# Performance work log

Measured on AMD Instinct MI355X. Metric: run time of the kernel, lower is better.

Reference implementation:

```python
import jax, jax.numpy as jnp
import numpy as np

EMBED_DIM = 4096
NUM_HEADS = 32
HEAD_DIM = EMBED_DIM // NUM_HEADS  # 128
KV_LEN = 8192


def setup_inputs() -> dict:
    key = jax.random.key(0)
    ks = jax.random.split(key, 12)
    s = 1.0 / np.sqrt(EMBED_DIM)
    return {
        "x": jax.random.normal(ks[0], (EMBED_DIM,), jnp.float32),
        "v": jax.random.normal(ks[1], (KV_LEN, NUM_HEADS, HEAD_DIM), jnp.float32),
        "k": jax.random.normal(ks[2], (KV_LEN, NUM_HEADS, HEAD_DIM), jnp.float32),
        "Wv": jax.random.normal(ks[3], (EMBED_DIM, EMBED_DIM), jnp.float32) * s,
        "bv": jnp.zeros((EMBED_DIM,), jnp.float32),
        "Wq": jax.random.normal(ks[4], (EMBED_DIM, EMBED_DIM), jnp.float32) * s,
        "bq": jnp.zeros((EMBED_DIM,), jnp.float32),
        "Wk": jax.random.normal(ks[5], (EMBED_DIM, EMBED_DIM), jnp.float32) * s,
        "bk": jnp.zeros((EMBED_DIM,), jnp.float32),
        "Wo": jax.random.normal(ks[6], (EMBED_DIM, EMBED_DIM), jnp.float32) * s,
        "bo": jnp.zeros((EMBED_DIM,), jnp.float32),
    }


def reference(x, v, k, Wv, bv, Wq, bq, Wk, bk, Wo, bo):
    # Project the single incoming token to q/k/v heads.
    v_i = (x @ Wv + bv).reshape(1, NUM_HEADS, HEAD_DIM)
    q_i = (x @ Wq + bq).reshape(NUM_HEADS, HEAD_DIM)
    k_i = (x @ Wk + bk).reshape(1, NUM_HEADS, HEAD_DIM)
    # Rolling cache: drop oldest slot, append new token.
    v = jnp.concatenate((v[1:], v_i), axis=0)  # [KV_LEN, H, D]
    k = jnp.concatenate((k[1:], k_i), axis=0)
    # Valid slots are those with any nonzero value entry.
    mask = jnp.any(v != 0, axis=(1, 2))  # [KV_LEN]
    attn = jnp.einsum('hd,khd->hk', q_i, k) / jnp.sqrt(jnp.float32(HEAD_DIM))
    attn = jnp.where(mask, attn, -jnp.inf)
    attn = jax.nn.softmax(attn, axis=-1)  # [H, KV_LEN]
    values = jnp.einsum('hk,khd->hd', attn, v).reshape(EMBED_DIM)
    out_i = values @ Wo + bo
    return (out_i, v, k)
```

## Files before the change

### kernel.cpp

```cpp
#include <hip/hip_runtime.h>

#define E 4096
#define H 32
#define L 8192
#define SCALE 0.08838834764831845f

typedef float fv4 __attribute__((ext_vector_type(4)));

__device__ __forceinline__ fv4 ntload4(const float* p) {
  return __builtin_nontemporal_load(reinterpret_cast<const fv4*>(p));
}
__device__ __forceinline__ void ntstore4(float* p, fv4 v) {
  __builtin_nontemporal_store(v, reinterpret_cast<fv4*>(p));
}

__global__ __launch_bounds__(256) void zero_ws(float* __restrict__ ws, int n) {
  int i = blockIdx.x * 256 + threadIdx.x;
  if (i < n) ws[i] = 0.f;
}

__global__ __launch_bounds__(256) void gemv_qkv(const float* __restrict__ x,
    const float* __restrict__ Wq, const float* __restrict__ Wk,
    const float* __restrict__ Wv, float* __restrict__ qacc,
    float* __restrict__ kacc, float* __restrict__ vacc) {
  int b = blockIdx.x;
  int mat = b >> 7;
  int rem = b & 127;
  int chunk = rem >> 2;
  int g = rem & 3;
  const float* W = (mat == 0) ? Wq : (mat == 1) ? Wk : Wv;
  float* accb = (mat == 0) ? qacc : (mat == 1) ? kacc : vacc;
  int rep = (b >> 2) & 3;
  float* acc = accb + (rep << 12);
  int t = threadIdx.x;
  int j = (g << 10) + (t << 2);
  float ax = 0.f, ay = 0.f, az = 0.f, aw = 0.f;
  int i0 = chunk << 7;
  #pragma unroll 8
  for (int r = 0; r < 128; ++r) {
    int i = i0 + r;
    float xi = x[i];
    const fv4 w4 = ntload4(W + (size_t)i * E + j);
    ax += xi * w4.x; ay += xi * w4.y; az += xi * w4.z; aw += xi * w4.w;
  }
  atomicAdd(acc + j + 0, ax);
  atomicAdd(acc + j + 1, ay);
  atomicAdd(acc + j + 2, az);
  atomicAdd(acc + j + 3, aw);
}

__device__ __forceinline__ void load_slot(int o, int t,
    const float* __restrict__ kin, const float* __restrict__ vin,
    const float* __restrict__ kacc, const float* __restrict__ vacc,
    const float* __restrict__ bk, const float* __restrict__ bv,
    fv4 k4[4], fv4 v4[4]) {
  if (o < L - 1) {
    const float* ks = kin + (size_t)(o + 1) * E;
    const float* vs = vin + (size_t)(o + 1) * E;
    #pragma unroll
    for (int c = 0; c < 4; ++c) {
      int e = (c << 10) + (t << 2);
      k4[c] = ntload4(ks + e);
      v4[c] = ntload4(vs + e);
    }
  } else {
    #pragma unroll
    for (int c = 0; c < 4; ++c) {
      int e = (c << 10) + (t << 2);
      fv4 ka = *reinterpret_cast<const fv4*>(kacc + e);
      fv4 va = *reinterpret_cast<const fv4*>(vacc + e);
      #pragma unroll
      for (int r = 1; r < 4; ++r) {
        ka += *reinterpret_cast<const fv4*>(kacc + (r << 12) + e);
        va += *reinterpret_cast<const fv4*>(vacc + (r << 12) + e);
      }
      k4[c] = ka + *reinterpret_cast<const fv4*>(bk + e);
      v4[c] = va + *reinterpret_cast<const fv4*>(bv + e);
    }
  }
}

template<int NSLOTS, bool PARTIAL>
__global__ __launch_bounds__(256) void kvpass(const float* __restrict__ kin,
    const float* __restrict__ vin,
    const float* __restrict__ bq, const float* __restrict__ bk,
    const float* __restrict__ bv,
    const float* __restrict__ qacc, const float* __restrict__ kacc,
    const float* __restrict__ vacc,
    float* __restrict__ kout, float* __restrict__ vout,
    float* __restrict__ nump, float* __restrict__ denp) {
  __shared__ float wlds[NSLOTS * 32];
  __shared__ int flags[NSLOTS];
  int t = threadIdx.x;
  for (int s = t; s < NSLOTS; s += 256) flags[s] = 0;
  fv4 q4[4];
  #pragma unroll
  for (int c = 0; c < 4; ++c) {
    int e = (c << 10) + (t << 2);
    fv4 qa = *reinterpret_cast<const fv4*>(qacc + e);
    #pragma unroll
    for (int r = 1; r < 4; ++r)
      qa += *reinterpret_cast<const fv4*>(qacc + (r << 12) + e);
    q4[c] = qa + *reinterpret_cast<const fv4*>(bq + e);
  }
  __syncthreads();

  float accx[4] = {0,0,0,0}, accy[4] = {0,0,0,0};
  float accz[4] = {0,0,0,0}, accw[4] = {0,0,0,0};
  int base = blockIdx.x * NSLOTS;

  fv4 kc[4], vc[4], kn[4], vn[4];
  load_slot(base, t, kin, vin, kacc, vacc, bk, bv, kc, vc);

  for (int s = 0; s < NSLOTS; ++s) {
    int o = base + s;
    if (s + 1 < NSLOTS)
      load_slot(o + 1, t, kin, vin, kacc, vacc, bk, bv, kn, vn);
    float* kd = kout + (size_t)o * E;
    float* vd = vout + (size_t)o * E;
    #pragma unroll
    for (int c = 0; c < 4; ++c) {
      int e = (c << 10) + (t << 2);
      ntstore4(kd + e, kc[c]);
      ntstore4(vd + e, vc[c]);
    }
    bool nz = false;
    #pragma unroll
    for (int c = 0; c < 4; ++c) {
      float pp = kc[c].x * q4[c].x + kc[c].y * q4[c].y +
                 kc[c].z * q4[c].z + kc[c].w * q4[c].w;
      #pragma unroll
      for (int off = 16; off >= 1; off >>= 1)
        pp += __shfl_xor(pp, off);
      float w = __expf(pp * SCALE);
      accx[c] += w * vc[c].x; accy[c] += w * vc[c].y;
      accz[c] += w * vc[c].z; accw[c] += w * vc[c].w;
      if ((t & 31) == 0) wlds[(s << 5) + (c << 3) + (t >> 5)] = w;
      nz = nz || vc[c].x != 0.f || vc[c].y != 0.f || vc[c].z != 0.f || vc[c].w != 0.f;
    }
    unsigned long long b = __ballot(nz);
    if ((t & 63) == 0 && b != 0ULL) atomicOr(&flags[s], 1);
    #pragma unroll
    for (int c = 0; c < 4; ++c) { kc[c] = kn[c]; vc[c] = vn[c]; }
  }
  if (PARTIAL) {
    float* np = nump + ((size_t)blockIdx.x << 12);
    #pragma unroll
    for (int c = 0; c < 4; ++c) {
      int e = (c << 10) + (t << 2);
      fv4 val = {accx[c], accy[c], accz[c], accw[c]};
      *reinterpret_cast<fv4*>(np + e) = val;
    }
  } else {
    float* np = nump + ((size_t)(blockIdx.x & 15) << 12);
    #pragma unroll
    for (int c = 0; c < 4; ++c) {
      int e = (c << 10) + (t << 2);
      atomicAdd(np + e + 0, accx[c]);
      atomicAdd(np + e + 1, accy[c]);
      atomicAdd(np + e + 2, accz[c]);
      atomicAdd(np + e + 3, accw[c]);
    }
  }
  __syncthreads();
  if (t < 32) {
    float d = 0.f;
    #pragma unroll
    for (int s = 0; s < NSLOTS; ++s)
      if (flags[s]) d += wlds[(s << 5) + t];
    if (PARTIAL) denp[blockIdx.x * 64 + t] = d;
    else atomicAdd(denp + (blockIdx.x & 15) * 64 + t, d);
  }
}

template<int NP>
__global__ __launch_bounds__(256) void merge(const float* __restrict__ nump,
    const float* __restrict__ denp, float* __restrict__ num,
    float* __restrict__ den) {
  int b = blockIdx.x;
  int t = threadIdx.x;
  if (b < 16) {
    int e = b * 256 + t;
    float s = 0.f;
    #pragma unroll 8
    for (int p = 0; p < NP; ++p) s += nump[((size_t)p << 12) + e];
    num[e] = s;
  } else {
    __shared__ float dl[8][32];
    int g = t >> 5, h = t & 31;
    float d = 0.f;
    for (int p = g; p < NP; p += 8) d += denp[p * 64 + h];
    dl[g][h] = d;
    __syncthreads();
    if (t < 32) {
      float s = 0.f;
      #pragma unroll
      for (int g2 = 0; g2 < 8; ++g2) s += dl[g2][t];
      den[t] = s;
    }
  }
}

__global__ __launch_bounds__(256) void gemv_out(const float* __restrict__ Wo,
    const float* __restrict__ bo, const float* __restrict__ num,
    const float* __restrict__ den, float* __restrict__ opart) {
  int b = blockIdx.x;
  int chunk = b >> 2;
  int g = b & 3;
  int t = threadIdx.x;
  int j = (g << 10) + (t << 2);
  __shared__ float vals[64];
  int i0 = chunk << 6;
  if (t < 64) vals[t] = num[i0 + t] / den[(i0 + t) >> 7];
  __syncthreads();
  float ax = 0.f, ay = 0.f, az = 0.f, aw = 0.f;
  #pragma unroll 4
  for (int r = 0; r < 64; ++r) {
    int i = i0 + r;
    float vi = vals[r];
    const fv4 w4 = ntload4(Wo + (size_t)i * E + j);
    ax += vi * w4.x; ay += vi * w4.y; az += vi * w4.z; aw += vi * w4.w;
  }
  if (chunk == 0) {
    const fv4 b4 = *reinterpret_cast<const fv4*>(bo + j);
    ax += b4.x; ay += b4.y; az += b4.z; aw += b4.w;
  }
  fv4 val = {ax, ay, az, aw};
  *reinterpret_cast<fv4*>(opart + (chunk << 12) + j) = val;
}

__global__ __launch_bounds__(256) void writeout(const float* __restrict__ opart,
                                                float* __restrict__ out) {
  int i = blockIdx.x * 256 + threadIdx.x;
  float s = 0.f;
  #pragma unroll 8
  for (int c = 0; c < 64; ++c) s += opart[(c << 12) + i];
  out[i] = s;
}

extern "C" void kernel_launch(void* const* d_in, const int* in_sizes, int n_in,
                              void* d_out, int out_size, void* d_ws, size_t ws_size,
                              hipStream_t stream) {
  const float* x   = (const float*)d_in[0];
  const float* vin = (const float*)d_in[1];
  const float* kin = (const float*)d_in[2];
  const float* Wv  = (const float*)d_in[3];
  const float* bv  = (const float*)d_in[4];
  const float* Wq  = (const float*)d_in[5];
  const float* bq  = (const float*)d_in[6];
  const float* Wk  = (const float*)d_in[7];
  const float* bk  = (const float*)d_in[8];
  const float* Wo  = (const float*)d_in[9];
  const float* bo  = (const float*)d_in[10];
  float* out  = (float*)d_out;
  float* vout = out + E;
  float* kout = vout + (size_t)L * E;
  float* ws   = (float*)d_ws;

  float* qacc = ws;
  float* kacc = ws + 16384;
  float* vacc = ws + 32768;
  const size_t bigFloats = 49152 + (size_t)256 * 4096 + 256 * 64 + 4096 + 64
                         + (size_t)64 * 4096;
  bool big = ws_size >= bigFloats * sizeof(float);

  float *nump, *denp, *num, *den, *opart;
  int zcount;
  if (big) {
    nump = ws + 49152;
    denp = nump + (size_t)256 * 4096;
    num  = denp + 256 * 64;
    den  = num + 4096;
    opart = den + 64;
    zcount = 49152;
  } else {
    nump = ws + 49152;
    denp = nump + 16 * 4096;
    num  = denp + 16 * 64;
    den  = num + 4096;
    opart = den + 64;
    zcount = 49152 + 16 * 4096 + 16 * 64;
  }

  zero_ws<<<(zcount + 255) / 256, 256, 0, stream>>>(ws, zcount);
  gemv_qkv<<<384, 256, 0, stream>>>(x, Wq, Wk, Wv, qacc, kacc, vacc);
  if (big) {
    kvpass<32, true><<<L / 32, 256, 0, stream>>>(kin, vin, bq, bk, bv,
        qacc, kacc, vacc, kout, vout, nump, denp);
    merge<256><<<17, 256, 0, stream>>>(nump, denp, num, den);
  } else {
    kvpass<16, false><<<L / 16, 256, 0, stream>>>(kin, vin, bq, bk, bv,
        qacc, kacc, vacc, kout, vout, nump, denp);
    merge<16><<<17, 256, 0, stream>>>(nump, denp, num, den);
  }
  gemv_out<<<256, 256, 0, stream>>>(Wo, bo, num, den, opart);
  writeout<<<16, 256, 0, stream>>>(opart, out);
}
```

Measured before the change: 191.8 us.

## Overlap K/V projection GEMV with KV-cache streaming pass in one kernel

Splits the QKV projection so only Q is computed first. The K and V projection blocks are appended to the KV streaming kernel, so their weight reads overlap with the cache copy and attention pass. The single new-token slot is handled by a separate one-block finish kernel. The KV loop is restructured into a two-buffer ping-pong with launch bounds set for 3 blocks per CU, and the large-workspace partial path is dropped in favor of 16-way atomic accumulation. The cost is an extra tiny serial launch and more atomics in exchange for removing the serial K/V GEMV stage.

Result: slower. 198.8 us (+3.6%).

```diff
diff --git a/kernel.cpp b/kernel.cpp
--- a/kernel.cpp
+++ b/kernel.cpp
@@ -14,33 +14,34 @@
   __builtin_nontemporal_store(v, reinterpret_cast<fv4*>(p));
 }
 
-__global__ __launch_bounds__(256) void zero_ws(float* __restrict__ ws, int n) {
+#define WS_QACC  0
+#define WS_KACC  16384
+#define WS_VACC  32768
+#define WS_NUMP  49152
+#define WS_DENP  114688
+#define WS_ZERO  115712
+#define WS_NUM   115712
+#define WS_DEN   119808
+#define WS_OPART 119872
+
+__global__ __launch_bounds__(256) void zero_ws(float* __restrict__ ws) {
   int i = blockIdx.x * 256 + threadIdx.x;
-  if (i < n) ws[i] = 0.f;
-}
-
-__global__ __launch_bounds__(256) void gemv_qkv(const float* __restrict__ x,
-    const float* __restrict__ Wq, const float* __restrict__ Wk,
-    const float* __restrict__ Wv, float* __restrict__ qacc,
-    float* __restrict__ kacc, float* __restrict__ vacc) {
+  if (i < WS_ZERO) ws[i] = 0.f;
+}
+
+__global__ __launch_bounds__(256) void gemv_q(const float* __restrict__ x,
+    const float* __restrict__ Wq, float* __restrict__ qacc) {
   int b = blockIdx.x;
-  int mat = b >> 7;
-  int rem = b & 127;
-  int chunk = rem >> 2;
-  int g = rem & 3;
-  const float* W = (mat == 0) ? Wq : (mat == 1) ? Wk : Wv;
-  float* accb = (mat == 0) ? qacc : (mat == 1) ? kacc : vacc;
-  int rep = (b >> 2) & 3;
-  float* acc = accb + (rep << 12);
-  int t = threadIdx.x;
+  int chunk = b >> 2, g = b & 3, t = threadIdx.x;
+  float* acc = qacc + ((chunk & 3) << 12);
   int j = (g << 10) + (t << 2);
   float ax = 0.f, ay = 0.f, az = 0.f, aw = 0.f;
-  int i0 = chunk << 7;
+  int i0 = chunk << 6;
   #pragma unroll 8
-  for (int r = 0; r < 128; ++r) {
+  for (int r = 0; r < 64; ++r) {
     int i = i0 + r;
     float xi = x[i];
-    const fv4 w4 = ntload4(W + (size_t)i * E + j);
+    const fv4 w4 = ntload4(Wq + (size_t)i * E + j);
     ax += xi * w4.x; ay += xi * w4.y; az += xi * w4.z; aw += xi * w4.w;
   }
   atomicAdd(acc + j + 0, ax);
@@ -49,131 +50,198 @@
   atomicAdd(acc + j + 3, aw);
 }
 
-__device__ __forceinline__ void load_slot(int o, int t,
+#define NSLOTS 16
+
+__device__ __forceinline__ void ld(int o, int t,
     const float* __restrict__ kin, const float* __restrict__ vin,
-    const float* __restrict__ kacc, const float* __restrict__ vacc,
-    const float* __restrict__ bk, const float* __restrict__ bv,
     fv4 k4[4], fv4 v4[4]) {
-  if (o < L - 1) {
-    const float* ks = kin + (size_t)(o + 1) * E;
-    const float* vs = vin + (size_t)(o + 1) * E;
-    #pragma unroll
-    for (int c = 0; c < 4; ++c) {
-      int e = (c << 10) + (t << 2);
-      k4[c] = ntload4(ks + e);
-      v4[c] = ntload4(vs + e);
+  const float* ks = kin + (size_t)(o + 1) * E;
+  const float* vs = vin + (size_t)(o + 1) * E;
+  #pragma unroll
+  for (int c = 0; c < 4; ++c) {
+    int e = (c << 10) + (t << 2);
+    k4[c] = ntload4(ks + e);
+    v4[c] = ntload4(vs + e);
+  }
+}
+
+__device__ __forceinline__ void proc(int o, int s, int t,
+    const fv4 k4[4], const fv4 v4[4], const fv4 q4[4],
+    float* __restrict__ kout, float* __restrict__ vout,
+    float accx[4], float accy[4], float accz[4], float accw[4],
+    float* wlds, int* flags) {
+  float* kd = kout + (size_t)o * E;
+  float* vd = vout + (size_t)o * E;
+  #pragma unroll
+  for (int c = 0; c < 4; ++c) {
+    int e = (c << 10) + (t << 2);
+    ntstore4(kd + e, k4[c]);
+    ntstore4(vd + e, v4[c]);
+  }
+  bool nz = false;
+  #pragma unroll
+  for (int c = 0; c < 4; ++c) {
+    float pp = k4[c].x * q4[c].x + k4[c].y * q4[c].y +
+               k4[c].z * q4[c].z + k4[c].w * q4[c].w;
+    #pragma unroll
+    for (int off = 16; off >= 1; off >>= 1)
+      pp += __shfl_xor(pp, off);
+    float w = __expf(pp * SCALE);
+    accx[c] += w * v4[c].x; accy[c] += w * v4[c].y;
+    accz[c] += w * v4[c].z; accw[c] += w * v4[c].w;
+    if ((t & 31) == 0) wlds[(s << 5) + (c << 3) + (t >> 5)] = w;
+    nz = nz || v4[c].x != 0.f || v4[c].y != 0.f || v4[c].z != 0.f || v4[c].w != 0.f;
+  }
+  unsigned long long b = __ballot(nz);
+  if ((t & 63) == 0 && b != 0ULL) atomicOr(&flags[s], 1);
+}
+
+__global__ __launch_bounds__(256, 3) void mega(
+    const float* __restrict__ kin, const float* __restrict__ vin,
+    const float* __restrict__ x,
+    const float* __restrict__ Wk, const float* __restrict__ Wv,
+    const float* __restrict__ bq, const float* __restrict__ qacc,
+    float* __restrict__ kacc, float* __restrict__ vacc,
+    float* __restrict__ kout, float* __restrict__ vout,
+    float* __restrict__ nump, float* __restrict__ denp) {
+  int bid = blockIdx.x;
+  int t = threadIdx.x;
+  if (bid >= 512) {
+    int b = bid - 512;
+    int mat = b >> 7, rem = b & 127;
+    int chunk = rem >> 2, g = rem & 3;
+    const float* W = mat ? Wv : Wk;
+    float* acc = (mat ? vacc : kacc) + ((chunk & 3) << 12);
+    int j = (g << 10) + (t << 2);
+    float ax = 0.f, ay = 0.f, az = 0.f, aw = 0.f;
+    int i0 = chunk << 7;
+    #pragma unroll 8
+    for (int r = 0; r < 128; ++r) {
+      int i = i0 + r;
+      float xi = x[i];
+      const fv4 w4 = ntload4(W + (size_t)i * E + j);
+      ax += xi * w4.x; ay += xi * w4.y; az += xi * w4.z; aw += xi * w4.w;
     }
-  } else {
-    #pragma unroll
-    for (int c = 0; c < 4; ++c) {
-      int e = (c << 10) + (t << 2);
-      fv4 ka = *reinterpret_cast<const fv4*>(kacc + e);
-      fv4 va = *reinterpret_cast<const fv4*>(vacc + e);
-      #pragma unroll
-      for (int r = 1; r < 4; ++r) {
-        ka += *reinterpret_cast<const fv4*>(kacc + (r << 12) + e);
-        va += *reinterpret_cast<const fv4*>(vacc + (r << 12) + e);
-      }
-      k4[c] = ka + *reinterpret_cast<const fv4*>(bk + e);
-      v4[c] = va + *reinterpret_cast<const fv4*>(bv + e);
-    }
-  }
-}
-
-template<int NSLOTS, bool PARTIAL>
-__global__ __launch_bounds__(256) void kvpass(const float* __restrict__ kin,
-    const float* __restrict__ vin,
+    atomicAdd(acc + j + 0, ax);
+    atomicAdd(acc + j + 1, ay);
+    atomicAdd(acc + j + 2, az);
+    atomicAdd(acc + j + 3, aw);
+    return;
+  }
+  __shared__ float wlds[NSLOTS * 32];
+  __shared__ int flags[NSLOTS];
+  for (int s = t; s < NSLOTS; s += 256) flags[s] = 0;
+  fv4 q4[4];
+  #pragma unroll
+  for (int c = 0; c < 4; ++c) {
+    int e = (c << 10) + (t << 2);
+    fv4 qa = *reinterpret_cast<const fv4*>(qacc + e);
+    #pragma unroll
+    for (int r = 1; r < 4; ++r)
+      qa += *reinterpret_cast<const fv4*>(qacc + (r << 12) + e);
+    q4[c] = qa + *reinterpret_cast<const fv4*>(bq + e);
+  }
+  __syncthreads();
+
+  float accx[4] = {0,0,0,0}, accy[4] = {0,0,0,0};
+  float accz[4] = {0,0,0,0}, accw[4] = {0,0,0,0};
+  int base = bid * NSLOTS;
+
+  fv4 kA[4], vA[4], kB[4], vB[4];
+  ld(base, t, kin, vin, kA, vA);
+  #pragma unroll
+  for (int sp = 0; sp < NSLOTS; sp += 2) {
+    int oB = base + sp + 1;
+    bool haveB = oB < L - 1;
+    if (haveB) ld(oB, t, kin, vin, kB, vB);
+    proc(base + sp, sp, t, kA, vA, q4, kout, vout, accx, accy, accz, accw,
+         wlds, flags);
+    if (sp + 2 < NSLOTS) ld(base + sp + 2, t, kin, vin, kA, vA);
+    if (haveB) proc(oB, sp + 1, t, kB, vB, q4, kout, vout, accx, accy,
+                    accz, accw, wlds, flags);
+  }
+  float* np = nump + ((size_t)(bid & 15) << 12);
+  #pragma unroll
+  for (int c = 0; c < 4; ++c) {
+    int e = (c << 10) + (t << 2);
+    atomicAdd(np + e + 0, accx[c]);
+    atomicAdd(np + e + 1, accy[c]);
+    atomicAdd(np + e + 2, accz[c]);
+    atomicAdd(np + e + 3, accw[c]);
+  }
+  __syncthreads();
+  if (t < 32) {
+    float d = 0.f;
+    #pragma unroll
+    for (int s = 0; s < NSLOTS; ++s)
+      if (flags[s]) d += wlds[(s << 5) + t];
+    atomicAdd(denp + (bid & 15) * 64 + t, d);
+  }
+}
+
+__global__ __launch_bounds__(256) void finish(
     const float* __restrict__ bq, const float* __restrict__ bk,
     const float* __restrict__ bv,
     const float* __restrict__ qacc, const float* __restrict__ kacc,
     const float* __restrict__ vacc,
     float* __restrict__ kout, float* __restrict__ vout,
     float* __restrict__ nump, float* __restrict__ denp) {
-  __shared__ float wlds[NSLOTS * 32];
-  __shared__ int flags[NSLOTS];
   int t = threadIdx.x;
-  for (int s = t; s < NSLOTS; s += 256) flags[s] = 0;
-  fv4 q4[4];
+  __shared__ float wl[32];
+  __shared__ int nzf;
+  if (t == 0) nzf = 0;
+  fv4 q4[4], k4[4], v4[4];
   #pragma unroll
   for (int c = 0; c < 4; ++c) {
     int e = (c << 10) + (t << 2);
     fv4 qa = *reinterpret_cast<const fv4*>(qacc + e);
-    #pragma unroll
-    for (int r = 1; r < 4; ++r)
+    fv4 ka = *reinterpret_cast<const fv4*>(kacc + e);
+    fv4 va = *reinterpret_cast<const fv4*>(vacc + e);
+    #pragma unroll
+    for (int r = 1; r < 4; ++r) {
       qa += *reinterpret_cast<const fv4*>(qacc + (r << 12) + e);
+      ka += *reinterpret_cast<const fv4*>(kacc + (r << 12) + e);
+      va += *reinterpret_cast<const fv4*>(vacc + (r << 12) + e);
+    }
     q4[c] = qa + *reinterpret_cast<const fv4*>(bq + e);
-  }
-  __syncthreads();
-
-  float accx[4] = {0,0,0,0}, accy[4] = {0,0,0,0};
-  float accz[4] = {0,0,0,0}, accw[4] = {0,0,0,0};
-  int base = blockIdx.x * NSLOTS;
-
-  fv4 kc[4], vc[4], kn[4], vn[4];
-  load_slot(base, t, kin, vin, kacc, vacc, bk, bv, kc, vc);
-
-  for (int s = 0; s < NSLOTS; ++s) {
-    int o = base + s;
-    if (s + 1 < NSLOTS)
-      load_slot(o + 1, t, kin, vin, kacc, vacc, bk, bv, kn, vn);
-    float* kd = kout + (size_t)o * E;
-    float* vd = vout + (size_t)o * E;
+    k4[c] = ka + *reinterpret_cast<const fv4*>(bk + e);
+    v4[c] = va + *reinterpret_cast<const fv4*>(bv + e);
+  }
+  __syncthreads();
+  float* kd = kout + (size_t)(L - 1) * E;
+  float* vd = vout + (size_t)(L - 1) * E;
+  bool nz = false;
+  float wv[4];
+  #pragma unroll
+  for (int c = 0; c < 4; ++c) {
+    int e = (c << 10) + (t << 2);
+    *reinterpret_cast<fv4*>(kd + e) = k4[c];
+    *reinterpret_cast<fv4*>(vd + e) = v4[c];
+    float pp = k4[c].x * q4[c].x + k4[c].y * q4[c].y +
+               k4[c].z * q4[c].z + k4[c].w * q4[c].w;
+    #pragma unroll
+    for (int off = 16; off >= 1; off >>= 1)
+      pp += __shfl_xor(pp, off);
+    wv[c] = __expf(pp * SCALE);
+    if ((t & 31) == 0) wl[(c << 3) + (t >> 5)] = wv[c];
+    nz = nz || v4[c].x != 0.f || v4[c].y != 0.f || v4[c].z != 0.f || v4[c].w != 0.f;
+  }
+  unsigned long long b = __ballot(nz);
+  if ((t & 63) == 0 && b != 0ULL) atomicOr(&nzf, 1);
+  __syncthreads();
+  if (nzf) {
     #pragma unroll
     for (int c = 0; c < 4; ++c) {
       int e = (c << 10) + (t << 2);
-      ntstore4(kd + e, kc[c]);
-      ntstore4(vd + e, vc[c]);
+      atomicAdd(nump + e + 0, wv[c] * v4[c].x);
+      atomicAdd(nump + e + 1, wv[c] * v4[c].y);
+      atomicAdd(nump + e + 2, wv[c] * v4[c].z);
+      atomicAdd(nump + e + 3, wv[c] * v4[c].w);
     }
-    bool nz = false;
-    #pragma unroll
-    for (int c = 0; c < 4; ++c) {
-      float pp = kc[c].x * q4[c].x + kc[c].y * q4[c].y +
-                 kc[c].z * q4[c].z + kc[c].w * q4[c].w;
-      #pragma unroll
-      for (int off = 16; off >= 1; off >>= 1)
-        pp += __shfl_xor(pp, off);
-      float w = __expf(pp * SCALE);
-      accx[c] += w * vc[c].x; accy[c] += w * vc[c].y;
-      accz[c] += w * vc[c].z; accw[c] += w * vc[c].w;
-      if ((t & 31) == 0) wlds[(s << 5) + (c << 3) + (t >> 5)] = w;
-      nz = nz || vc[c].x != 0.f || vc[c].y != 0.f || vc[c].z != 0.f || vc[c].w != 0.f;
-    }
-    unsigned long long b = __ballot(nz);
-    if ((t & 63) == 0 && b != 0ULL) atomicOr(&flags[s], 1);
-    #pragma unroll
-    for (int c = 0; c < 4; ++c) { kc[c] = kn[c]; vc[c] = vn[c]; }
-  }
-  if (PARTIAL) {
-    float* np = nump + ((size_t)blockIdx.x << 12);
-    #pragma unroll
-    for (int c = 0; c < 4; ++c) {
-      int e = (c << 10) + (t << 2);
-      fv4 val = {accx[c], accy[c], accz[c], accw[c]};
-      *reinterpret_cast<fv4*>(np + e) = val;
-    }
-  } else {
-    float* np = nump + ((size_t)(blockIdx.x & 15) << 12);
-    #pragma unroll
-    for (int c = 0; c < 4; ++c) {
-      int e = (c << 10) + (t << 2);
-      atomicAdd(np + e + 0, accx[c]);
-      atomicAdd(np + e + 1, accy[c]);
-      atomicAdd(np + e + 2, accz[c]);
-      atomicAdd(np + e + 3, accw[c]);
-    }
-  }
-  __syncthreads();
-  if (t < 32) {
-    float d = 0.f;
-    #pragma unroll
-    for (int s = 0; s < NSLOTS; ++s)
-      if (flags[s]) d += wlds[(s << 5) + t];
-    if (PARTIAL) denp[blockIdx.x * 64 + t] = d;
-    else atomicAdd(denp + (blockIdx.x & 15) * 64 + t, d);
-  }
-}
-
-template<int NP>
+    if (t < 32) atomicAdd(denp + t, wl[t]);
+  }
+}
+
 __global__ __launch_bounds__(256) void merge(const float* __restrict__ nump,
     const float* __restrict__ denp, float* __restrict__ num,
     float* __restrict__ den) {
@@ -182,14 +250,14 @@
   if (b < 16) {
     int e = b * 256 + t;
     float s = 0.f;
-    #pragma unroll 8
-    for (int p = 0; p < NP; ++p) s += nump[((size_t)p << 12) + e];
+    #pragma unroll
+    for (int p = 0; p < 16; ++p) s += nump[((size_t)p << 12) + e];
     num[e] = s;
   } else {
     __shared__ float dl[8][32];
     int g = t >> 5, h = t & 31;
     float d = 0.f;
-    for (int p = g; p < NP; p += 8) d += denp[p * 64 + h];
+    for (int p = g; p < 16; p += 8) d += denp[p * 64 + h];
     dl[g][h] = d;
     __syncthreads();
     if (t < 32) {
@@ -205,9 +273,7 @@
     const float* __restrict__ bo, const float* __restrict__ num,
     const float* __restrict__ den, float* __restrict__ opart) {
   int b = blockIdx.x;
-  int chunk = b >> 2;
-  int g = b & 3;
-  int t = threadIdx.x;
+  int chunk = b >> 2, g = b & 3, t = threadIdx.x;
   int j = (g << 10) + (t << 2);
   __shared__ float vals[64];
   int i0 = chunk << 6;
@@ -257,42 +323,22 @@
   float* kout = vout + (size_t)L * E;
   float* ws   = (float*)d_ws;
 
-  float* qacc = ws;
-  float* kacc = ws + 16384;
-  float* vacc = ws + 32768;
-  const size_t bigFloats = 49152 + (size_t)256 * 4096 + 256 * 64 + 4096 + 64
-                         + (size_t)64 * 4096;
-  bool big = ws_size >= bigFloats * sizeof(float);
-
-  float *nump, *denp, *num, *den, *opart;
-  int zcount;
-  if (big) {
-    nump = ws + 49152;
-    denp = nump + (size_t)256 * 4096;
-    num  = denp + 256 * 64;
-    den  = num + 4096;
-    opart = den + 64;
-    zcount = 49152;
-  } else {
-    nump = ws + 49152;
-    denp = nump + 16 * 4096;
-    num  = denp + 16 * 64;
-    den  = num + 4096;
-    opart = den + 64;
-    zcount = 49152 + 16 * 4096 + 16 * 64;
-  }
-
-  zero_ws<<<(zcount + 255) / 256, 256, 0, stream>>>(ws, zcount);
-  gemv_qkv<<<384, 256, 0, stream>>>(x, Wq, Wk, Wv, qacc, kacc, vacc);
-  if (big) {
-    kvpass<32, true><<<L / 32, 256, 0, stream>>>(kin, vin, bq, bk, bv,
-        qacc, kacc, vacc, kout, vout, nump, denp);
-    merge<256><<<17, 256, 0, stream>>>(nump, denp, num, den);
-  } else {
-    kvpass<16, false><<<L / 16, 256, 0, stream>>>(kin, vin, bq, bk, bv,
-        qacc, kacc, vacc, kout, vout, nump, denp);
-    merge<16><<<17, 256, 0, stream>>>(nump, denp, num, den);
-  }
+  float* qacc = ws + WS_QACC;
+  float* kacc = ws + WS_KACC;
+  float* vacc = ws + WS_VACC;
+  float* nump = ws + WS_NUMP;
+  float* denp = ws + WS_DENP;
+  float* num  = ws + WS_NUM;
+  float* den  = ws + WS_DEN;
+  float* opart = ws + WS_OPART;
+
+  zero_ws<<<(WS_ZERO + 255) / 256, 256, 0, stream>>>(ws);
+  gemv_q<<<256, 256, 0, stream>>>(x, Wq, qacc);
+  mega<<<768, 256, 0, stream>>>(kin, vin, x, Wk, Wv, bq, qacc, kacc, vacc,
+                                kout, vout, nump, denp);
+  finish<<<1, 256, 0, stream>>>(bq, bk, bv, qacc, kacc, vacc,
+                                kout, vout, nump, denp);
+  merge<<<17, 256, 0, stream>>>(nump, denp, num, den);
   gemv_out<<<256, 256, 0, stream>>>(Wo, bo, num, den, opart);
   writeout<<<16, 256, 0, stream>>>(opart, out);
 }
```
